# Performance work log

Measured on AMD Instinct MI355X. Metric: run time of the kernel, lower is better.

Reference implementation:

```python
import jax, jax.numpy as jnp
import numpy as np

N_NODES = 50000
N_EDGES = 800000
IN_DIM = 96
HID = 96


def setup_inputs() -> dict:
    key = jax.random.key(0)
    k1, k2, k3, k4 = jax.random.split(key, 4)
    x = jax.random.normal(k1, (N_NODES, IN_DIM), dtype=jnp.float32)
    edge_index = jax.random.randint(k2, (2, N_EDGES), 0, N_NODES, dtype=jnp.int64)
    s1 = 1.0 / np.sqrt(IN_DIM)
    s2 = 1.0 / np.sqrt(HID)
    W1 = jax.random.normal(k3, (IN_DIM, HID), dtype=jnp.float32) * s1
    b1 = jnp.zeros((HID,), dtype=jnp.float32)
    W2 = jax.random.normal(k4, (HID, HID), dtype=jnp.float32) * s2
    b2 = jnp.zeros((HID,), dtype=jnp.float32)
    return {"x": x, "edge_index": edge_index, "W1": W1, "b1": b1, "W2": W2, "b2": b2}


def _gcn_conv(x, src, dst, norm, W, b, n_nodes):
    # x' = D^{-1/2}(A+I)D^{-1/2} X W + b  (PyG GCNConv semantics)
    xw = x @ W                           # [N, out]
    msg = xw[src] * norm[:, None]        # gather + edge-normalize, [E+N, out]
    agg = jax.ops.segment_sum(msg, dst, num_segments=n_nodes)  # scatter-add
    return agg + b


def reference(x, edge_index, W1, b1, W2, b2):
    n_nodes = x.shape[0]
    loops = jnp.arange(n_nodes, dtype=edge_index.dtype)
    src = jnp.concatenate([edge_index[0], loops])  # sources (j)
    dst = jnp.concatenate([edge_index[1], loops])  # targets (i), aggregation index
    # symmetric normalization with self-loops; degree counted at targets
    deg = jax.ops.segment_sum(jnp.ones(dst.shape, dtype=x.dtype), dst, num_segments=n_nodes)
    dinv = jnp.where(deg > 0, jax.lax.rsqrt(deg), 0.0)
    norm = dinv[src] * dinv[dst]
    h = jax.nn.relu(_gcn_conv(x, src, dst, norm, W1, b1, n_nodes))
    h = jax.nn.relu(_gcn_conv(h, src, dst, norm, W2, b2, n_nodes))
    return h
```

## Files before the change

### kernel.cpp

```cpp
#include <hip/hip_runtime.h>

#define N_NODES 50000
#define N_EDGES 800000
#define DIM 96
#define FEAT_ELEMS (N_NODES * DIM)
#define NBLK 196
#define EGRID 3125
#define CGRID 4688
#define GGRID 782
#define APAD 104

typedef __attribute__((ext_vector_type(8))) short short8;
typedef __attribute__((ext_vector_type(4))) float float4v;

__device__ __forceinline__ float bf16_to_f32(unsigned short u) {
    unsigned int w = ((unsigned int)u) << 16;
    float f;
    __builtin_memcpy(&f, &w, 4);
    return f;
}
__device__ __forceinline__ unsigned short f32_to_bf16_rne(float f) {
    unsigned int w;
    __builtin_memcpy(&w, &f, 4);
    unsigned int r = (w + 0x7FFFu + ((w >> 16) & 1u)) >> 16;
    return (unsigned short)r;
}
__device__ __forceinline__ unsigned int pack_bf16x2(float lo, float hi) {
    return (unsigned int)f32_to_bf16_rne(lo) | ((unsigned int)f32_to_bf16_rne(hi) << 16);
}

__device__ __forceinline__ int edge_at(const void* ep, int is64, int idx) {
    if (is64) return (int)((const long long*)ep)[idx];
    return ((const int*)ep)[idx];
}

__global__ __launch_bounds__(256) void prolog_kernel(const unsigned int* edges,
                                                     const unsigned int* x,
                                                     int* flagE, int* flagF, int* cnt) {
    __shared__ unsigned int sh[256];
    int t = threadIdx.x;
    int b = blockIdx.x;
    if (b < NBLK) {
        int i = b * 256 + t;
        if (i < N_NODES) cnt[i] = 0;
        return;
    }
    if (b == NBLK) {
        if (t < 64) {
            unsigned int acc = 0;
            for (int k = 0; k < 4; ++k) {
                int idx = t * 4 + k;
                int pos = 1 + 2 * idx * 3109;
                acc |= edges[pos];
            }
            sh[t] = acc;
        }
        __syncthreads();
        if (t == 0) {
            unsigned int a = 0;
            for (int i = 0; i < 64; ++i) a |= sh[i];
            *flagE = (a == 0u) ? 1 : 0;
        }
        return;
    }
    unsigned int w = x[t * 9000];
    unsigned int e = (w >> 7) & 0xFFu;
    sh[t] = (e >= 100u && e <= 135u) ? 1u : 0u;
    __syncthreads();
    if (t == 0) {
        int c = 0;
        for (int i = 0; i < 256; ++i) c += (int)sh[i];
        *flagF = (c >= 128) ? 1 : 0;
    }
}

__global__ __launch_bounds__(256) void count_convert_kernel(const void* __restrict__ edges,
                                                            const void* __restrict__ x,
                                                            const int* __restrict__ flagE,
                                                            const int* __restrict__ flagF,
                                                            int* __restrict__ cnt,
                                                            unsigned short* __restrict__ srcu,
                                                            unsigned short* __restrict__ dstu,
                                                            unsigned short* __restrict__ rank,
                                                            unsigned short* __restrict__ xb) {
    int b = blockIdx.x;
    if (b < EGRID) {
        int e = b * 256 + threadIdx.x;
        int is64 = *flagE;
        int s = edge_at(edges, is64, e);
        int d = edge_at(edges, is64, N_EDGES + e);
        srcu[e] = (unsigned short)s;
        dstu[e] = (unsigned short)d;
        rank[e] = (unsigned short)atomicAdd(&cnt[d], 1);
        return;
    }
    int i4 = ((b - EGRID) * 256 + threadIdx.x) * 4;
    if (i4 >= FEAT_ELEMS) return;
    int isbf16 = *flagF;
    ushort4 o;
    if (isbf16) {
        o = *(const ushort4*)((const unsigned short*)x + i4);
    } else {
        float4 v = *(const float4*)((const float*)x + i4);
        o.x = f32_to_bf16_rne(v.x);
        o.y = f32_to_bf16_rne(v.y);
        o.z = f32_to_bf16_rne(v.z);
        o.w = f32_to_bf16_rne(v.w);
    }
    *(ushort4*)(xb + i4) = o;
}

__global__ __launch_bounds__(256) void scan_blocksum_kernel(const int* cnt, int* blockSums) {
    __shared__ int sh[256];
    int i = blockIdx.x * 256 + threadIdx.x;
    sh[threadIdx.x] = (i < N_NODES) ? cnt[i] : 0;
    __syncthreads();
    for (int off = 128; off > 0; off >>= 1) {
        if (threadIdx.x < off) sh[threadIdx.x] += sh[threadIdx.x + off];
        __syncthreads();
    }
    if (threadIdx.x == 0) blockSums[blockIdx.x] = sh[0];
}

__global__ __launch_bounds__(256) void scan_apply_kernel(const int* __restrict__ cnt,
                                                         const int* __restrict__ blockSums,
                                                         int* __restrict__ row_ptr,
                                                         float* __restrict__ dinv) {
    __shared__ int sb[256];
    __shared__ int sh[256];
    int t = threadIdx.x;
    sb[t] = (t < NBLK) ? blockSums[t] : 0;
    __syncthreads();
    for (int off = 1; off < 256; off <<= 1) {
        int u = (t >= off) ? sb[t - off] : 0;
        __syncthreads();
        sb[t] += u;
        __syncthreads();
    }
    int b = blockIdx.x;
    int blockOff = (b == 0) ? 0 : sb[b - 1];
    if (b == 0 && t == 0) row_ptr[N_NODES] = sb[NBLK - 1];

    int i = b * 256 + t;
    int c = (i < N_NODES) ? cnt[i] : 0;
    sh[t] = c;
    __syncthreads();
    for (int off = 1; off < 256; off <<= 1) {
        int u = (t >= off) ? sh[t - off] : 0;
        __syncthreads();
        sh[t] += u;
        __syncthreads();
    }
    if (i < N_NODES) {
        row_ptr[i] = sh[t] - c + blockOff;
        dinv[i]    = rsqrtf((float)(c + 1));
    }
}

__global__ __launch_bounds__(256) void fill_direct_kernel(const unsigned short* __restrict__ dstu,
                                                          const unsigned short* __restrict__ srcu,
                                                          const unsigned short* __restrict__ rank,
                                                          const int* __restrict__ row_ptr,
                                                          unsigned short* __restrict__ csr_src) {
    int e = blockIdx.x * 256 + threadIdx.x;
    if (e >= N_EDGES) return;
    int d = dstu[e];
    int pos = row_ptr[d] + (int)rank[e];
    csr_src[pos] = srcu[e];
}

__global__ __launch_bounds__(256) void fused_layer_kernel(const unsigned short* __restrict__ feat,
                                                          const int* __restrict__ row_ptr,
                                                          const unsigned short* __restrict__ csr_src,
                                                          const float* __restrict__ dinv,
                                                          const void* __restrict__ W,
                                                          const void* __restrict__ bias,
                                                          const int* __restrict__ flagF,
                                                          void* __restrict__ out, int outMode) {
    __shared__ __align__(16) unsigned short Wsw[3 * 6 * 64 * 8];
    __shared__ __align__(16) unsigned short Atile[64 * APAD];

    int t = threadIdx.x;
    int wBf16 = *flagF;
    int outBf16 = (outMode == 2) ? wBf16 : outMode;

    for (int f = t; f < 1152; f += 256) {
        int kt = f / 384;
        int rem = f - kt * 384;
        int nt = rem >> 6;
        int ln64 = rem & 63;
        int q = ln64 >> 4, ln = ln64 & 15;
        int k0 = kt * 32 + q * 8;
        int n = nt * 16 + ln;
        unsigned short e[8];
        if (wBf16) {
            const unsigned short* Wh = (const unsigned short*)W;
            #pragma unroll
            for (int j = 0; j < 8; ++j) e[j] = Wh[(k0 + j) * DIM + n];
        } else {
            const float* Wf = (const float*)W;
            #pragma unroll
            for (int j = 0; j < 8; ++j) e[j] = f32_to_bf16_rne(Wf[(k0 + j) * DIM + n]);
        }
        uint4 pk;
        pk.x = (unsigned int)e[0] | ((unsigned int)e[1] << 16);
        pk.y = (unsigned int)e[2] | ((unsigned int)e[3] << 16);
        pk.z = (unsigned int)e[4] | ((unsigned int)e[5] << 16);
        pk.w = (unsigned int)e[6] | ((unsigned int)e[7] << 16);
        *(uint4*)&Wsw[f * 8] = pk;
    }

    int m0 = blockIdx.x * 64;
    int grp = t >> 4;
    int l = t & 15;
    for (int p = 0; p < 4; ++p) {
        int r = grp * 4 + p;
        int g = m0 + r;
        float a0 = 0.f, a1 = 0.f, a2 = 0.f, a3 = 0.f, a4 = 0.f, a5 = 0.f;
        if (g < N_NODES) {
            float di = dinv[g];
            int gb = g * DIM + l * 2;
            ushort2 sv0 = *(const ushort2*)&feat[gb];
            ushort2 sv1 = *(const ushort2*)&feat[gb + 32];
            ushort2 sv2 = *(const ushort2*)&feat[gb + 64];
            float wself = di * di;
            a0 = wself * bf16_to_f32(sv0.x); a1 = wself * bf16_to_f32(sv0.y);
            a2 = wself * bf16_to_f32(sv1.x); a3 = wself * bf16_to_f32(sv1.y);
            a4 = wself * bf16_to_f32(sv2.x); a5 = wself * bf16_to_f32(sv2.y);
            int e = row_ptr[g], e1 = row_ptr[g + 1];
            for (; e + 2 <= e1; e += 2) {
                int s0 = csr_src[e];
                int s1 = csr_src[e + 1];
                float w0 = dinv[s0] * di;
                float w1 = dinv[s1] * di;
                int b0 = s0 * DIM + l * 2;
                int b1 = s1 * DIM + l * 2;
                ushort2 p0 = *(const ushort2*)&feat[b0];
                ushort2 p1 = *(const ushort2*)&feat[b0 + 32];
                ushort2 p2 = *(const ushort2*)&feat[b0 + 64];
                ushort2 q0 = *(const ushort2*)&feat[b1];
                ushort2 q1 = *(const ushort2*)&feat[b1 + 32];
                ushort2 q2 = *(const ushort2*)&feat[b1 + 64];
                a0 = fmaf(w0, bf16_to_f32(p0.x), a0);  a1 = fmaf(w0, bf16_to_f32(p0.y), a1);
                a2 = fmaf(w0, bf16_to_f32(p1.x), a2);  a3 = fmaf(w0, bf16_to_f32(p1.y), a3);
                a4 = fmaf(w0, bf16_to_f32(p2.x), a4);  a5 = fmaf(w0, bf16_to_f32(p2.y), a5);
                a0 = fmaf(w1, bf16_to_f32(q0.x), a0);  a1 = fmaf(w1, bf16_to_f32(q0.y), a1);
                a2 = fmaf(w1, bf16_to_f32(q1.x), a2);  a3 = fmaf(w1, bf16_to_f32(q1.y), a3);
                a4 = fmaf(w1, bf16_to_f32(q2.x), a4);  a5 = fmaf(w1, bf16_to_f32(q2.y), a5);
            }
            if (e < e1) {
                int s = csr_src[e];
                float w = dinv[s] * di;
                int b0 = s * DIM + l * 2;
                ushort2 p0 = *(const ushort2*)&feat[b0];
                ushort2 p1 = *(const ushort2*)&feat[b0 + 32];
                ushort2 p2 = *(const ushort2*)&feat[b0 + 64];
                a0 = fmaf(w, bf16_to_f32(p0.x), a0);  a1 = fmaf(w, bf16_to_f32(p0.y), a1);
                a2 = fmaf(w, bf16_to_f32(p1.x), a2);  a3 = fmaf(w, bf16_to_f32(p1.y), a3);
                a4 = fmaf(w, bf16_to_f32(p2.x), a4);  a5 = fmaf(w, bf16_to_f32(p2.y), a5);
            }
        }
        int ab = r * APAD + l * 2;
        *(unsigned int*)&Atile[ab]      = pack_bf16x2(a0, a1);
        *(unsigned int*)&Atile[ab + 32] = pack_bf16x2(a2, a3);
        *(unsigned int*)&Atile[ab + 64] = pack_bf16x2(a4, a5);
    }
    __syncthreads();

    int wave = t >> 6;
    int lane = t & 63;
    int quad = lane >> 4, ln = lane & 15;
    int rloc = wave * 16 + ln;

    float4v acc[6];
    #pragma unroll
    for (int nt = 0; nt < 6; ++nt) acc[nt] = (float4v){0.f, 0.f, 0.f, 0.f};

    #pragma unroll
    for (int kt = 0; kt < 3; ++kt) {
        short8 af = *(const short8*)&Atile[rloc * APAD + kt * 32 + quad * 8];
        #pragma unroll
        for (int nt = 0; nt < 6; ++nt) {
            short8 bf = *(const short8*)&Wsw[((kt * 6 + nt) * 64 + lane) * 8];
            acc[nt] = __builtin_amdgcn_mfma_f32_16x16x32_bf16(af, bf, acc[nt], 0, 0, 0);
        }
    }

    #pragma unroll
    for (int nt = 0; nt < 6; ++nt) {
        int n = nt * 16 + ln;
        float bv = wBf16 ? bf16_to_f32(((const unsigned short*)bias)[n])
                         : ((const float*)bias)[n];
        #pragma unroll
        for (int reg = 0; reg < 4; ++reg) {
            int row = m0 + wave * 16 + quad * 4 + reg;
            if (row >= N_NODES) continue;
            float v = fmaxf(acc[nt][reg] + bv, 0.0f);
            if (outBf16) ((unsigned short*)out)[row * DIM + n] = f32_to_bf16_rne(v);
            else         ((float*)out)[row * DIM + n] = v;
        }
    }
}

extern "C" void kernel_launch(void* const* d_in, const int* in_sizes, int n_in,
                              void* d_out, int out_size, void* d_ws, size_t ws_size,
                              hipStream_t stream) {
    const void* x  = d_in[0];
    const void* ei = d_in[1];
    const void* W1 = d_in[2];
    const void* b1 = d_in[3];
    const void* W2 = d_in[4];
    const void* b2 = d_in[5];

    char* base = (char*)d_ws;
    size_t off = 0;
    auto carve = [&](size_t bytes) -> void* {
        void* p = base + off;
        off += (bytes + 255) & ~(size_t)255;
        return p;
    };
    int*            flagE     = (int*)carve(4);
    int*            flagF     = (int*)carve(4);
    int*            cnt       = (int*)carve((size_t)N_NODES * 4);
    int*            row_ptr   = (int*)carve((size_t)(N_NODES + 1) * 4);
    float*          dinv      = (float*)carve((size_t)N_NODES * 4);
    int*            blockSums = (int*)carve((size_t)NBLK * 4);
    unsigned short* srcu      = (unsigned short*)carve((size_t)N_EDGES * 2);
    unsigned short* dstu      = (unsigned short*)carve((size_t)N_EDGES * 2);
    unsigned short* rank      = (unsigned short*)carve((size_t)N_EDGES * 2);
    unsigned short* csr_src   = (unsigned short*)carve((size_t)N_EDGES * 2);
    unsigned short* xb        = (unsigned short*)carve((size_t)FEAT_ELEMS * 2);
    unsigned short* h         = (unsigned short*)carve((size_t)FEAT_ELEMS * 2);

    prolog_kernel<<<NBLK + 2, 256, 0, stream>>>((const unsigned int*)ei,
                                                (const unsigned int*)x, flagE, flagF, cnt);
    count_convert_kernel<<<EGRID + CGRID, 256, 0, stream>>>(ei, x, flagE, flagF, cnt,
                                                            srcu, dstu, rank, xb);
    scan_blocksum_kernel<<<NBLK, 256, 0, stream>>>(cnt, blockSums);
    scan_apply_kernel<<<NBLK, 256, 0, stream>>>(cnt, blockSums, row_ptr, dinv);
    fill_direct_kernel<<<EGRID, 256, 0, stream>>>(dstu, srcu, rank, row_ptr, csr_src);

    fused_layer_kernel<<<GGRID, 256, 0, stream>>>(xb, row_ptr, csr_src, dinv,
                                                  W1, b1, flagF, h, 1);
    fused_layer_kernel<<<GGRID, 256, 0, stream>>>(h, row_ptr, csr_src, dinv,
                                                  W2, b2, flagF, d_out, 2);
}
```

Measured before the change: 230.6 us.

## Split fused aggregate+GEMM into high-occupancy gather and standalone MFMA GEMM kernels

Each layer's fused kernel is split into a gather kernel, with one 16-thread group per node, and a separate MFMA GEMM kernel that reads the aggregated bf16 rows from global memory. Per-edge normalization weights are precomputed into a csr_w array during CSR fill. Weight swizzling moves into the convert kernel, so it runs once instead of in every GEMM block. The aim is more parallelism and latency hiding in the gather, which previously ran as 782 blocks each walking 4 nodes per group serially. The cost is an extra round trip of the aggregated feature matrix through memory, an extra float per edge, and two more launches.

New measurement: 217.4 us. -5.7%, faster.

```diff
diff --git a/kernel.cpp b/kernel.cpp
--- a/kernel.cpp
+++ b/kernel.cpp
@@ -7,8 +7,9 @@
 #define NBLK 196
 #define EGRID 3125
 #define CGRID 4688
+#define WGRID 10
+#define AGRID 3125
 #define GGRID 782
-#define APAD 104
 
 typedef __attribute__((ext_vector_type(8))) short short8;
 typedef __attribute__((ext_vector_type(4))) float float4v;
@@ -76,13 +77,17 @@
 
 __global__ __launch_bounds__(256) void count_convert_kernel(const void* __restrict__ edges,
                                                             const void* __restrict__ x,
+                                                            const void* __restrict__ W1,
+                                                            const void* __restrict__ W2,
                                                             const int* __restrict__ flagE,
                                                             const int* __restrict__ flagF,
                                                             int* __restrict__ cnt,
                                                             unsigned short* __restrict__ srcu,
                                                             unsigned short* __restrict__ dstu,
                                                             unsigned short* __restrict__ rank,
-                                                            unsigned short* __restrict__ xb) {
+                                                            unsigned short* __restrict__ xb,
+                                                            unsigned short* __restrict__ wsw1,
+                                                            unsigned short* __restrict__ wsw2) {
     int b = blockIdx.x;
     if (b < EGRID) {
         int e = b * 256 + threadIdx.x;
@@ -94,20 +99,53 @@
         rank[e] = (unsigned short)atomicAdd(&cnt[d], 1);
         return;
     }
-    int i4 = ((b - EGRID) * 256 + threadIdx.x) * 4;
-    if (i4 >= FEAT_ELEMS) return;
-    int isbf16 = *flagF;
-    ushort4 o;
-    if (isbf16) {
-        o = *(const ushort4*)((const unsigned short*)x + i4);
+    if (b < EGRID + CGRID) {
+        int i4 = ((b - EGRID) * 256 + threadIdx.x) * 4;
+        if (i4 >= FEAT_ELEMS) return;
+        int isbf16 = *flagF;
+        ushort4 o;
+        if (isbf16) {
+            o = *(const ushort4*)((const unsigned short*)x + i4);
+        } else {
+            float4 v = *(const float4*)((const float*)x + i4);
+            o.x = f32_to_bf16_rne(v.x);
+            o.y = f32_to_bf16_rne(v.y);
+            o.z = f32_to_bf16_rne(v.z);
+            o.w = f32_to_bf16_rne(v.w);
+        }
+        *(ushort4*)(xb + i4) = o;
+        return;
+    }
+    int wi = b - EGRID - CGRID;
+    int which = wi / 5;
+    int f = (wi - which * 5) * 256 + threadIdx.x;
+    if (f >= 1152) return;
+    const void* Wp = which ? W2 : W1;
+    unsigned short* Op = which ? wsw2 : wsw1;
+    int wBf16 = *flagF;
+    int kt = f / 384;
+    int rem = f - kt * 384;
+    int nt = rem >> 6;
+    int ln64 = rem & 63;
+    int q = ln64 >> 4, ln = ln64 & 15;
+    int k0 = kt * 32 + q * 8;
+    int n = nt * 16 + ln;
+    unsigned short e[8];
+    if (wBf16) {
+        const unsigned short* Wh = (const unsigned short*)Wp;
+        #pragma unroll
+        for (int j = 0; j < 8; ++j) e[j] = Wh[(k0 + j) * DIM + n];
     } else {
-        float4 v = *(const float4*)((const float*)x + i4);
-        o.x = f32_to_bf16_rne(v.x);
-        o.y = f32_to_bf16_rne(v.y);
-        o.z = f32_to_bf16_rne(v.z);
-        o.w = f32_to_bf16_rne(v.w);
-    }
-    *(ushort4*)(xb + i4) = o;
+        const float* Wf = (const float*)Wp;
+        #pragma unroll
+        for (int j = 0; j < 8; ++j) e[j] = f32_to_bf16_rne(Wf[(k0 + j) * DIM + n]);
+    }
+    uint4 pk;
+    pk.x = (unsigned int)e[0] | ((unsigned int)e[1] << 16);
+    pk.y = (unsigned int)e[2] | ((unsigned int)e[3] << 16);
+    pk.z = (unsigned int)e[4] | ((unsigned int)e[5] << 16);
+    pk.w = (unsigned int)e[6] | ((unsigned int)e[7] << 16);
+    *(uint4*)&Op[f * 8] = pk;
 }
 
 __global__ __launch_bounds__(256) void scan_blocksum_kernel(const int* cnt, int* blockSums) {
@@ -161,116 +199,106 @@
                                                           const unsigned short* __restrict__ srcu,
                                                           const unsigned short* __restrict__ rank,
                                                           const int* __restrict__ row_ptr,
-                                                          unsigned short* __restrict__ csr_src) {
+                                                          const float* __restrict__ dinv,
+                                                          unsigned short* __restrict__ csr_src,
+                                                          float* __restrict__ csr_w) {
     int e = blockIdx.x * 256 + threadIdx.x;
     if (e >= N_EDGES) return;
     int d = dstu[e];
+    int s = srcu[e];
     int pos = row_ptr[d] + (int)rank[e];
-    csr_src[pos] = srcu[e];
-}
-
-__global__ __launch_bounds__(256) void fused_layer_kernel(const unsigned short* __restrict__ feat,
-                                                          const int* __restrict__ row_ptr,
-                                                          const unsigned short* __restrict__ csr_src,
-                                                          const float* __restrict__ dinv,
-                                                          const void* __restrict__ W,
-                                                          const void* __restrict__ bias,
-                                                          const int* __restrict__ flagF,
-                                                          void* __restrict__ out, int outMode) {
-    __shared__ __align__(16) unsigned short Wsw[3 * 6 * 64 * 8];
-    __shared__ __align__(16) unsigned short Atile[64 * APAD];
-
-    int t = threadIdx.x;
+    csr_src[pos] = (unsigned short)s;
+    csr_w[pos]   = dinv[s] * dinv[d];
+}
+
+__global__ __launch_bounds__(256) void gather_kernel(const unsigned short* __restrict__ feat,
+                                                     const int* __restrict__ row_ptr,
+                                                     const unsigned short* __restrict__ csr_src,
+                                                     const float* __restrict__ csr_w,
+                                                     const float* __restrict__ dinv,
+                                                     unsigned short* __restrict__ aggb) {
+    int gid = blockIdx.x * 256 + threadIdx.x;
+    int g = gid >> 4;
+    int l = gid & 15;
+    if (g >= N_NODES) return;
+    float di = dinv[g];
+    int gb = g * DIM + l * 2;
+    ushort2 sv0 = *(const ushort2*)&feat[gb];
+    ushort2 sv1 = *(const ushort2*)&feat[gb + 32];
+    ushort2 sv2 = *(const ushort2*)&feat[gb + 64];
+    float wself = di * di;
+    float a0 = wself * bf16_to_f32(sv0.x), a1 = wself * bf16_to_f32(sv0.y);
+    float a2 = wself * bf16_to_f32(sv1.x), a3 = wself * bf16_to_f32(sv1.y);
+    float a4 = wself * bf16_to_f32(sv2.x), a5 = wself * bf16_to_f32(sv2.y);
+    int e = row_ptr[g], e1 = row_ptr[g + 1];
+    for (; e + 4 <= e1; e += 4) {
+        int s0 = csr_src[e + 0];
+        int s1 = csr_src[e + 1];
+        int s2 = csr_src[e + 2];
+        int s3 = csr_src[e + 3];
+        float w0 = csr_w[e + 0];
+        float w1 = csr_w[e + 1];
+        float w2 = csr_w[e + 2];
+        float w3 = csr_w[e + 3];
+        int b0 = s0 * DIM + l * 2;
+        int b1 = s1 * DIM + l * 2;
+        int b2 = s2 * DIM + l * 2;
+        int b3 = s3 * DIM + l * 2;
+        ushort2 p0 = *(const ushort2*)&feat[b0];
+        ushort2 p1 = *(const ushort2*)&feat[b0 + 32];
+        ushort2 p2 = *(const ushort2*)&feat[b0 + 64];
+        ushort2 q0 = *(const ushort2*)&feat[b1];
+        ushort2 q1 = *(const ushort2*)&feat[b1 + 32];
+        ushort2 q2 = *(const ushort2*)&feat[b1 + 64];
+        ushort2 r0 = *(const ushort2*)&feat[b2];
+        ushort2 r1 = *(const ushort2*)&feat[b2 + 32];
+        ushort2 r2 = *(const ushort2*)&feat[b2 + 64];
+        ushort2 t0 = *(const ushort2*)&feat[b3];
+        ushort2 t1 = *(const ushort2*)&feat[b3 + 32];
+        ushort2 t2 = *(const ushort2*)&feat[b3 + 64];
+        a0 = fmaf(w0, bf16_to_f32(p0.x), a0);  a1 = fmaf(w0, bf16_to_f32(p0.y), a1);
+        a2 = fmaf(w0, bf16_to_f32(p1.x), a2);  a3 = fmaf(w0, bf16_to_f32(p1.y), a3);
+        a4 = fmaf(w0, bf16_to_f32(p2.x), a4);  a5 = fmaf(w0, bf16_to_f32(p2.y), a5);
+        a0 = fmaf(w1, bf16_to_f32(q0.x), a0);  a1 = fmaf(w1, bf16_to_f32(q0.y), a1);
+        a2 = fmaf(w1, bf16_to_f32(q1.x), a2);  a3 = fmaf(w1, bf16_to_f32(q1.y), a3);
+        a4 = fmaf(w1, bf16_to_f32(q2.x), a4);  a5 = fmaf(w1, bf16_to_f32(q2.y), a5);
+        a0 = fmaf(w2, bf16_to_f32(r0.x), a0);  a1 = fmaf(w2, bf16_to_f32(r0.y), a1);
+        a2 = fmaf(w2, bf16_to_f32(r1.x), a2);  a3 = fmaf(w2, bf16_to_f32(r1.y), a3);
+        a4 = fmaf(w2, bf16_to_f32(r2.x), a4);  a5 = fmaf(w2, bf16_to_f32(r2.y), a5);
+        a0 = fmaf(w3, bf16_to_f32(t0.x), a0);  a1 = fmaf(w3, bf16_to_f32(t0.y), a1);
+        a2 = fmaf(w3, bf16_to_f32(t1.x), a2);  a3 = fmaf(w3, bf16_to_f32(t1.y), a3);
+        a4 = fmaf(w3, bf16_to_f32(t2.x), a4);  a5 = fmaf(w3, bf16_to_f32(t2.y), a5);
+    }
+    for (; e < e1; ++e) {
+        int s = csr_src[e];
+        float w = csr_w[e];
+        int b0 = s * DIM + l * 2;
+        ushort2 p0 = *(const ushort2*)&feat[b0];
+        ushort2 p1 = *(const ushort2*)&feat[b0 + 32];
+        ushort2 p2 = *(const ushort2*)&feat[b0 + 64];
+        a0 = fmaf(w, bf16_to_f32(p0.x), a0);  a1 = fmaf(w, bf16_to_f32(p0.y), a1);
+        a2 = fmaf(w, bf16_to_f32(p1.x), a2);  a3 = fmaf(w, bf16_to_f32(p1.y), a3);
+        a4 = fmaf(w, bf16_to_f32(p2.x), a4);  a5 = fmaf(w, bf16_to_f32(p2.y), a5);
+    }
+    *(unsigned int*)&aggb[gb]      = pack_bf16x2(a0, a1);
+    *(unsigned int*)&aggb[gb + 32] = pack_bf16x2(a2, a3);
+    *(unsigned int*)&aggb[gb + 64] = pack_bf16x2(a4, a5);
+}
+
+__global__ __launch_bounds__(256) void gemm_mfma_kernel(const unsigned short* __restrict__ A,
+                                                        const unsigned short* __restrict__ Wsw,
+                                                        const void* __restrict__ bias,
+                                                        const int* __restrict__ flagF,
+                                                        void* __restrict__ out, int outMode) {
     int wBf16 = *flagF;
     int outBf16 = (outMode == 2) ? wBf16 : outMode;
-
-    for (int f = t; f < 1152; f += 256) {
-        int kt = f / 384;
-        int rem = f - kt * 384;
-        int nt = rem >> 6;
-        int ln64 = rem & 63;
-        int q = ln64 >> 4, ln = ln64 & 15;
-        int k0 = kt * 32 + q * 8;
-        int n = nt * 16 + ln;
-        unsigned short e[8];
-        if (wBf16) {
-            const unsigned short* Wh = (const unsigned short*)W;
-            #pragma unroll
-            for (int j = 0; j < 8; ++j) e[j] = Wh[(k0 + j) * DIM + n];
-        } else {
-            const float* Wf = (const float*)W;
-            #pragma unroll
-            for (int j = 0; j < 8; ++j) e[j] = f32_to_bf16_rne(Wf[(k0 + j) * DIM + n]);
-        }
-        uint4 pk;
-        pk.x = (unsigned int)e[0] | ((unsigned int)e[1] << 16);
-        pk.y = (unsigned int)e[2] | ((unsigned int)e[3] << 16);
-        pk.z = (unsigned int)e[4] | ((unsigned int)e[5] << 16);
-        pk.w = (unsigned int)e[6] | ((unsigned int)e[7] << 16);
-        *(uint4*)&Wsw[f * 8] = pk;
-    }
-
-    int m0 = blockIdx.x * 64;
-    int grp = t >> 4;
-    int l = t & 15;
-    for (int p = 0; p < 4; ++p) {
-        int r = grp * 4 + p;
-        int g = m0 + r;
-        float a0 = 0.f, a1 = 0.f, a2 = 0.f, a3 = 0.f, a4 = 0.f, a5 = 0.f;
-        if (g < N_NODES) {
-            float di = dinv[g];
-            int gb = g * DIM + l * 2;
-            ushort2 sv0 = *(const ushort2*)&feat[gb];
-            ushort2 sv1 = *(const ushort2*)&feat[gb + 32];
-            ushort2 sv2 = *(const ushort2*)&feat[gb + 64];
-            float wself = di * di;
-            a0 = wself * bf16_to_f32(sv0.x); a1 = wself * bf16_to_f32(sv0.y);
-            a2 = wself * bf16_to_f32(sv1.x); a3 = wself * bf16_to_f32(sv1.y);
-            a4 = wself * bf16_to_f32(sv2.x); a5 = wself * bf16_to_f32(sv2.y);
-            int e = row_ptr[g], e1 = row_ptr[g + 1];
-            for (; e + 2 <= e1; e += 2) {
-                int s0 = csr_src[e];
-                int s1 = csr_src[e + 1];
-                float w0 = dinv[s0] * di;
-                float w1 = dinv[s1] * di;
-                int b0 = s0 * DIM + l * 2;
-                int b1 = s1 * DIM + l * 2;
-                ushort2 p0 = *(const ushort2*)&feat[b0];
-                ushort2 p1 = *(const ushort2*)&feat[b0 + 32];
-                ushort2 p2 = *(const ushort2*)&feat[b0 + 64];
-                ushort2 q0 = *(const ushort2*)&feat[b1];
-                ushort2 q1 = *(const ushort2*)&feat[b1 + 32];
-                ushort2 q2 = *(const ushort2*)&feat[b1 + 64];
-                a0 = fmaf(w0, bf16_to_f32(p0.x), a0);  a1 = fmaf(w0, bf16_to_f32(p0.y), a1);
-                a2 = fmaf(w0, bf16_to_f32(p1.x), a2);  a3 = fmaf(w0, bf16_to_f32(p1.y), a3);
-                a4 = fmaf(w0, bf16_to_f32(p2.x), a4);  a5 = fmaf(w0, bf16_to_f32(p2.y), a5);
-                a0 = fmaf(w1, bf16_to_f32(q0.x), a0);  a1 = fmaf(w1, bf16_to_f32(q0.y), a1);
-                a2 = fmaf(w1, bf16_to_f32(q1.x), a2);  a3 = fmaf(w1, bf16_to_f32(q1.y), a3);
-                a4 = fmaf(w1, bf16_to_f32(q2.x), a4);  a5 = fmaf(w1, bf16_to_f32(q2.y), a5);
-            }
-            if (e < e1) {
-                int s = csr_src[e];
-                float w = dinv[s] * di;
-                int b0 = s * DIM + l * 2;
-                ushort2 p0 = *(const ushort2*)&feat[b0];
-                ushort2 p1 = *(const ushort2*)&feat[b0 + 32];
-                ushort2 p2 = *(const ushort2*)&feat[b0 + 64];
-                a0 = fmaf(w, bf16_to_f32(p0.x), a0);  a1 = fmaf(w, bf16_to_f32(p0.y), a1);
-                a2 = fmaf(w, bf16_to_f32(p1.x), a2);  a3 = fmaf(w, bf16_to_f32(p1.y), a3);
-                a4 = fmaf(w, bf16_to_f32(p2.x), a4);  a5 = fmaf(w, bf16_to_f32(p2.y), a5);
-            }
-        }
-        int ab = r * APAD + l * 2;
-        *(unsigned int*)&Atile[ab]      = pack_bf16x2(a0, a1);
-        *(unsigned int*)&Atile[ab + 32] = pack_bf16x2(a2, a3);
-        *(unsigned int*)&Atile[ab + 64] = pack_bf16x2(a4, a5);
-    }
-    __syncthreads();
-
+    int t = threadIdx.x;
     int wave = t >> 6;
     int lane = t & 63;
     int quad = lane >> 4, ln = lane & 15;
-    int rloc = wave * 16 + ln;
+    int m0 = blockIdx.x * 64 + wave * 16;
+    int arow = m0 + ln;
+    bool arowok = (arow < N_NODES);
 
     float4v acc[6];
     #pragma unroll
@@ -278,7 +306,12 @@
 
     #pragma unroll
     for (int kt = 0; kt < 3; ++kt) {
-        short8 af = *(const short8*)&Atile[rloc * APAD + kt * 32 + quad * 8];
+        short8 af;
+        if (arowok) {
+            af = *(const short8*)&A[arow * DIM + kt * 32 + quad * 8];
+        } else {
+            af = (short8){0, 0, 0, 0, 0, 0, 0, 0};
+        }
         #pragma unroll
         for (int nt = 0; nt < 6; ++nt) {
             short8 bf = *(const short8*)&Wsw[((kt * 6 + nt) * 64 + lane) * 8];
@@ -293,7 +326,7 @@
                          : ((const float*)bias)[n];
         #pragma unroll
         for (int reg = 0; reg < 4; ++reg) {
-            int row = m0 + wave * 16 + quad * 4 + reg;
+            int row = m0 + quad * 4 + reg;
             if (row >= N_NODES) continue;
             float v = fmaxf(acc[nt][reg] + bv, 0.0f);
             if (outBf16) ((unsigned short*)out)[row * DIM + n] = f32_to_bf16_rne(v);
@@ -329,19 +362,25 @@
     unsigned short* dstu      = (unsigned short*)carve((size_t)N_EDGES * 2);
     unsigned short* rank      = (unsigned short*)carve((size_t)N_EDGES * 2);
     unsigned short* csr_src   = (unsigned short*)carve((size_t)N_EDGES * 2);
+    float*          csr_w     = (float*)carve((size_t)N_EDGES * 4);
+    unsigned short* wsw1      = (unsigned short*)carve((size_t)1152 * 8 * 2);
+    unsigned short* wsw2      = (unsigned short*)carve((size_t)1152 * 8 * 2);
+    unsigned short* aggb      = (unsigned short*)carve((size_t)FEAT_ELEMS * 2);
     unsigned short* xb        = (unsigned short*)carve((size_t)FEAT_ELEMS * 2);
     unsigned short* h         = (unsigned short*)carve((size_t)FEAT_ELEMS * 2);
 
     prolog_kernel<<<NBLK + 2, 256, 0, stream>>>((const unsigned int*)ei,
                                                 (const unsigned int*)x, flagE, flagF, cnt);
-    count_convert_kernel<<<EGRID + CGRID, 256, 0, stream>>>(ei, x, flagE, flagF, cnt,
-                                                            srcu, dstu, rank, xb);
+    count_convert_kernel<<<EGRID + CGRID + WGRID, 256, 0, stream>>>(
+        ei, x, W1, W2, flagE, flagF, cnt, srcu, dstu, rank, xb, wsw1, wsw2);
     scan_blocksum_kernel<<<NBLK, 256, 0, stream>>>(cnt, blockSums);
     scan_apply_kernel<<<NBLK, 256, 0, stream>>>(cnt, blockSums, row_ptr, dinv);
-    fill_direct_kernel<<<EGRID, 256, 0, stream>>>(dstu, srcu, rank, row_ptr, csr_src);
-
-    fused_layer_kernel<<<GGRID, 256, 0, stream>>>(xb, row_ptr, csr_src, dinv,
-                                                  W1, b1, flagF, h, 1);
-    fused_layer_kernel<<<GGRID, 256, 0, stream>>>(h, row_ptr, csr_src, dinv,
-                                                  W2, b2, flagF, d_out, 2);
-}
+    fill_direct_kernel<<<EGRID, 256, 0, stream>>>(dstu, srcu, rank, row_ptr, dinv,
+                                                  csr_src, csr_w);
+
+    gather_kernel<<<AGRID, 256, 0, stream>>>(xb, row_ptr, csr_src, csr_w, dinv, aggb);
+    gemm_mfma_kernel<<<GGRID, 256, 0, stream>>>(aggb, wsw1, b1, flagF, h, 1);
+
+    gather_kernel<<<AGRID, 256, 0, stream>>>(h, row_ptr, csr_src, csr_w, dinv, aggb);
+    gemm_mfma_kernel<<<GGRID, 256, 0, stream>>>(aggb, wsw2, b2, flagF, d_out, 2);
+}
```
